# Kernel tuning notes

Hardware: AMD Instinct MI355X
Metric: run time of the kernel (lower is better)

Reference implementation:

```python
import jax, jax.numpy as jnp
import numpy as np

HEADS = 8
GROUPS = 8  # min(8, ch)
EPS = 1e-5


def group_norm(x, gamma, beta):
    # x: (B, C, H, W); normalize over (C/G, H, W) per group
    B, C, H, W = x.shape
    xg = x.reshape(B, GROUPS, C // GROUPS, H, W)
    mu = jnp.mean(xg, axis=(2, 3, 4), keepdims=True)
    var = jnp.var(xg, axis=(2, 3, 4), keepdims=True)
    xn = ((xg - mu) * jax.lax.rsqrt(var + EPS)).reshape(B, C, H, W)
    return xn * gamma[None, :, None, None] + beta[None, :, None, None]


def setup_inputs() -> dict:
    key = jax.random.key(0)
    k1, k2, k3 = jax.random.split(key, 3)
    B, C, H, W = 8, 512, 32, 32
    x = jax.random.normal(k1, (B, C, H, W), dtype=jnp.float32)
    gn_gamma = jnp.ones((C,), dtype=jnp.float32)
    gn_beta = jnp.zeros((C,), dtype=jnp.float32)
    # conv1x1 weights, torch shape (out,in,1,1) squeezed to (out,in)
    w_qkv = jax.random.normal(k2, (3 * C, C), dtype=jnp.float32) * (1.0 / np.sqrt(C))
    w_proj = jax.random.normal(k3, (C, C), dtype=jnp.float32) * (1.0 / np.sqrt(C))
    b_proj = jnp.zeros((C,), dtype=jnp.float32)
    return {"x": x, "gn_gamma": gn_gamma, "gn_beta": gn_beta,
            "w_qkv": w_qkv, "w_proj": w_proj, "b_proj": b_proj}


def reference(x, gn_gamma, gn_beta, w_qkv, w_proj, b_proj):
    B, C, H, W = x.shape
    hd = C // HEADS  # head_dim
    N = H * W
    xn = group_norm(x, gn_gamma, gn_beta)
    # 1x1 conv == channel matmul: (B,3C,H,W)
    qkv = jnp.einsum('oc,bchw->bohw', w_qkv, xn)
    q, k, v = jnp.split(qkv, 3, axis=1)

    def sh(t):  # (B,C,H,W) -> (B, heads, N, head_dim)
        return t.reshape(B, HEADS, hd, N).transpose(0, 1, 3, 2)

    q, k, v = sh(q), sh(k), sh(v)
    scale = hd ** -0.5
    attn = jax.nn.softmax(jnp.einsum('bhnd,bhmd->bhnm', q, k) * scale, axis=-1)
    out = jnp.einsum('bhnm,bhmd->bhnd', attn, v)  # (B,heads,N,hd)
    out = out.transpose(0, 1, 3, 2).reshape(B, C, H, W)
    proj = jnp.einsum('oc,bchw->bohw', w_proj, out) + b_proj[None, :, None, None]
    return x + proj
```

## Files before the change

### kernel.cpp

```cpp
#include <hip/hip_runtime.h>
#include <cstdint>


typedef __bf16 bf16_t;
typedef bf16_t bf16x8 __attribute__((ext_vector_type(8)));
typedef float f32x4 __attribute__((ext_vector_type(4)));

__device__ __forceinline__ uint16_t f2bf(float f) {
  uint32_t x = __builtin_bit_cast(uint32_t, f);
  x += 0x7FFFu + ((x >> 16) & 1u);
  return (uint16_t)(x >> 16);
}
__device__ __forceinline__ bf16x8 frag_ld(const uint16_t* p) {
  return __builtin_bit_cast(bf16x8, *(const uint4*)p);
}
__device__ __forceinline__ void gl_lds16(const uint16_t* g, uint16_t* l) {
  __builtin_amdgcn_global_load_lds(
      (const __attribute__((address_space(1))) uint32_t*)g,
      (__attribute__((address_space(3))) uint32_t*)l, 16, 0, 0);
}
#define MFMA16(a, b, c) __builtin_amdgcn_mfma_f32_16x16x32_bf16((a), (b), (c), 0, 0, 0)

__global__ __launch_bounds__(256) void gnfused_k(const float* __restrict__ wq,
                                                 const float* __restrict__ wp,
                                                 uint16_t* __restrict__ wqb,
                                                 uint16_t* __restrict__ wpb,
                                                 const float* __restrict__ x,
                                                 const float* __restrict__ gamma,
                                                 const float* __restrict__ beta,
                                                 uint16_t* __restrict__ xn) {
  __shared__ alignas(16) float r1[256];
  __shared__ alignas(16) float r2[256];
  __shared__ alignas(16) uint16_t tile[64][72];
  __shared__ float smu, srstd;
  int bx = blockIdx.x, t = threadIdx.x;
  if (bx < 512) {
    int idx = (bx * 256 + t) * 8;
    const float* s;
    uint16_t* d;
    if (idx < 786432) { s = wq + idx; d = wqb + idx; }
    else              { s = wp + (idx - 786432); d = wpb + (idx - 786432); }
    float4 a = *(const float4*)s;
    float4 b = *(const float4*)(s + 4);
    union { uint16_t u[8]; uint4 v; } o;
    o.u[0] = f2bf(a.x); o.u[1] = f2bf(a.y); o.u[2] = f2bf(a.z); o.u[3] = f2bf(a.w);
    o.u[4] = f2bf(b.x); o.u[5] = f2bf(b.y); o.u[6] = f2bf(b.z); o.u[7] = f2bf(b.w);
    *(uint4*)d = o.v;
    return;
  }
  int bg = bx - 512;
  int b = bg >> 3, g = bg & 7;
  const float* xbase = x + (size_t)bg * 65536;

  {
    const float4* p4 = (const float4*)xbase;
    float s1 = 0.f, s2 = 0.f;
    for (int i = t; i < 16384; i += 256) {
      float4 u = p4[i];
      s1 += u.x + u.y + u.z + u.w;
      s2 += u.x * u.x + u.y * u.y + u.z * u.z + u.w * u.w;
    }
    r1[t] = s1; r2[t] = s2; __syncthreads();
    for (int o = 128; o > 0; o >>= 1) {
      if (t < o) { r1[t] += r1[t + o]; r2[t] += r2[t + o]; }
      __syncthreads();
    }
    if (t == 0) {
      float mu = r1[0] * (1.0f / 65536.0f);
      float var = r2[0] * (1.0f / 65536.0f) - mu * mu;
      smu = mu; srstd = rsqrtf(var + 1e-5f);
    }
    __syncthreads();
  }
  float mu = smu, rstd = srstd;

  int c_loc = t >> 2, nch = (t & 3) * 16;
  int c = g * 64 + c_loc;
  float gm = gamma[c], bt = beta[c];
  const float* srcc = xbase + (size_t)c_loc * 1024;
  int n_loc = t >> 2, c0 = (t & 3) * 16;
  uint16_t* dstc = xn + (size_t)b * 524288 + g * 64 + c0;
  for (int nt = 0; nt < 16; nt++) {
    int n0 = nt * 64;
    {
      const float* src = srcc + n0 + nch;
#pragma unroll
      for (int hh = 0; hh < 2; hh++) {
        float4 u0 = *(const float4*)(src + hh * 8);
        float4 u1 = *(const float4*)(src + hh * 8 + 4);
        union { uint16_t u16[8]; uint4 v; } o;
        o.u16[0] = f2bf((u0.x - mu) * rstd * gm + bt);
        o.u16[1] = f2bf((u0.y - mu) * rstd * gm + bt);
        o.u16[2] = f2bf((u0.z - mu) * rstd * gm + bt);
        o.u16[3] = f2bf((u0.w - mu) * rstd * gm + bt);
        o.u16[4] = f2bf((u1.x - mu) * rstd * gm + bt);
        o.u16[5] = f2bf((u1.y - mu) * rstd * gm + bt);
        o.u16[6] = f2bf((u1.z - mu) * rstd * gm + bt);
        o.u16[7] = f2bf((u1.w - mu) * rstd * gm + bt);
        *(uint4*)&tile[c_loc][nch + hh * 8] = o.v;
      }
    }
    __syncthreads();
    {
      union { uint16_t u16[16]; uint4 v[2]; } o;
#pragma unroll
      for (int j = 0; j < 16; j++) o.u16[j] = tile[c0 + j][n_loc];
      uint16_t* dst = dstc + (size_t)(n0 + n_loc) * 512;
      *(uint4*)dst = o.v[0];
      *(uint4*)(dst + 8) = o.v[1];
    }
    __syncthreads();
  }
}

template <int MODE>
__device__ __forceinline__ void gemm_body(uint16_t* Sh,
                                          const uint16_t* Arow, const uint16_t* Brow,
                                          uint16_t* O0, uint16_t* O1,
                                          int b, int n0, int o0) {
  uint16_t* As = Sh;
  uint16_t* Bs = Sh + 8192;
  int t = threadIdx.x;
  int lane = t & 63, w = t >> 6;
  int qd = lane >> 4, l15 = lane & 15;
  int wm = w & 1, wn = w >> 1;

  const uint16_t* gA[4];
  const uint16_t* gB[4];
  uint16_t* lA[4];
  uint16_t* lB[4];
#pragma unroll
  for (int i = 0; i < 4; i++) {
    int p = i * 256 + t;
    int row = p >> 3, slot = p & 7, gc = slot ^ (row & 7);
    gA[i] = Arow + (size_t)row * 512 + gc * 8;
    gB[i] = Brow + (size_t)row * 512 + gc * 8;
    lA[i] = As + (size_t)(p - lane) * 8;
    lB[i] = Bs + (size_t)(p - lane) * 8;
  }

  f32x4 acc[4][4] = {};

  for (int k0 = 0; k0 < 512; k0 += 64) {
    __syncthreads();
#pragma unroll
    for (int i = 0; i < 4; i++) { gl_lds16(gA[i] + k0, lA[i]); gl_lds16(gB[i] + k0, lB[i]); }
    __syncthreads();

#pragma unroll
    for (int h = 0; h < 2; h++) {
      int slot = (h * 4 + qd) ^ (l15 & 7);
      bf16x8 af[4], bfr[4];
#pragma unroll
      for (int mt = 0; mt < 4; mt++)
        af[mt] = frag_ld(As + (wm * 64 + mt * 16 + l15) * 64 + slot * 8);
#pragma unroll
      for (int nt2 = 0; nt2 < 4; nt2++)
        bfr[nt2] = frag_ld(Bs + (wn * 64 + nt2 * 16 + l15) * 64 + slot * 8);
#pragma unroll
      for (int mt = 0; mt < 4; mt++)
#pragma unroll
        for (int nt2 = 0; nt2 < 4; nt2++)
          acc[mt][nt2] = MFMA16(af[mt], bfr[nt2], acc[mt][nt2]);
    }
  }

  __syncthreads();
  uint16_t* buf = Sh + w * 1152;
  float sc = 1.0f;
  uint16_t* gbase;
  size_t rstride;
  int coff;
  if constexpr (MODE == 0) {
    int oc = o0 + wn * 64;
    int hh;
    uint16_t* db;
    if (oc < 512) { db = O0; hh = oc >> 6; sc = 0.125f; }
    else          { db = O1; hh = (oc - 512) >> 6; }
    gbase = db + (size_t)(b * 8 + hh) * 65536 + (size_t)(n0 + wm * 64) * 64;
    rstride = 64;  coff = 0;
  } else {
    gbase = O0 + (size_t)b * 524288 + (size_t)(o0 + wm * 64) * 1024;
    rstride = 1024; coff = n0 + wn * 64;
  }
  int jrow = lane >> 3, joff = (lane & 7) * 8;
#pragma unroll
  for (int mt = 0; mt < 4; mt++) {
#pragma unroll
    for (int nt2 = 0; nt2 < 4; nt2++)
#pragma unroll
      for (int r = 0; r < 4; r++)
        buf[(qd * 4 + r) * 72 + nt2 * 16 + l15] = f2bf(acc[mt][nt2][r] * sc);
#pragma unroll
    for (int half = 0; half < 2; half++) {
      int row = jrow + half * 8;
      uint4 v = *(const uint4*)(buf + row * 72 + joff);
      *(uint4*)(gbase + (size_t)(mt * 16 + row) * rstride + coff + joff) = v;
    }
  }
}

__global__ __launch_bounds__(256) void gemm01_k(const uint16_t* __restrict__ xn,
                                                const uint16_t* __restrict__ wqb,
                                                uint16_t* __restrict__ qtw,
                                                uint16_t* __restrict__ ktw,
                                                uint16_t* __restrict__ vtw) {
  __shared__ alignas(16) uint16_t Sh[16384];
  int id = blockIdx.x;
  int lo = id & 7, hi = id >> 3;
  int o12 = hi % 12, b = hi / 12;
  int n0 = lo * 128;
  if (o12 < 8) {
    int o0 = o12 * 128;
    gemm_body<0>(Sh, xn + (size_t)b * 524288 + (size_t)n0 * 512,
                 wqb + (size_t)o0 * 512, qtw, ktw, b, n0, o0);
  } else {
    int o0 = (o12 - 8) * 128;
    gemm_body<1>(Sh, wqb + (size_t)(1024 + o0) * 512,
                 xn + (size_t)b * 524288 + (size_t)n0 * 512, vtw, nullptr, b, n0, o0);
  }
}

__global__ __launch_bounds__(256) void gemm2_k(const uint16_t* __restrict__ wpb,
                                               const uint16_t* __restrict__ otw,
                                               const float* __restrict__ xres,
                                               const float* __restrict__ biasf,
                                               float* __restrict__ out) {
  __shared__ alignas(16) uint16_t As[2][8192];
  __shared__ alignas(16) uint16_t Bs[2][8192];
  int id = blockIdx.x;
  int lo = id & 7, hi = id >> 3;
  int o0 = (hi & 3) * 128, b = hi >> 2, n0 = lo * 128;
  const uint16_t* Arow = wpb + (size_t)o0 * 512;
  const uint16_t* Brow = otw + (size_t)b * 524288 + (size_t)n0 * 512;

  int t = threadIdx.x, lane = t & 63, w = t >> 6;
  int qd = lane >> 4, l15 = lane & 15;
  int wm = w & 1, wn = w >> 1;

  const uint16_t* gA[4];
  const uint16_t* gB[4];
  int lofs[4];
#pragma unroll
  for (int i = 0; i < 4; i++) {
    int p = i * 256 + t;
    int row = p >> 3, slot = p & 7, gc = slot ^ (row & 7);
    gA[i] = Arow + (size_t)row * 512 + gc * 8;
    gB[i] = Brow + (size_t)row * 512 + gc * 8;
    lofs[i] = (p - lane) * 8;
  }

  f32x4 acc[4][4] = {};
#pragma unroll
  for (int i = 0; i < 4; i++) { gl_lds16(gA[i], &As[0][lofs[i]]); gl_lds16(gB[i], &Bs[0][lofs[i]]); }
  __syncthreads();

  for (int kt = 0; kt < 8; kt++) {
    int cur = kt & 1, nxt = cur ^ 1;
    if (kt < 7) {
      int k0 = (kt + 1) * 64;
#pragma unroll
      for (int i = 0; i < 4; i++) { gl_lds16(gA[i] + k0, &As[nxt][lofs[i]]); gl_lds16(gB[i] + k0, &Bs[nxt][lofs[i]]); }
    }
#pragma unroll
    for (int h = 0; h < 2; h++) {
      int slot = (h * 4 + qd) ^ (l15 & 7);
      bf16x8 af[4], bfr[4];
#pragma unroll
      for (int mt = 0; mt < 4; mt++)
        af[mt] = frag_ld(&As[cur][(wm * 64 + mt * 16 + l15) * 64 + slot * 8]);
#pragma unroll
      for (int nt2 = 0; nt2 < 4; nt2++)
        bfr[nt2] = frag_ld(&Bs[cur][(wn * 64 + nt2 * 16 + l15) * 64 + slot * 8]);
#pragma unroll
      for (int mt = 0; mt < 4; mt++)
#pragma unroll
        for (int nt2 = 0; nt2 < 4; nt2++)
          acc[mt][nt2] = MFMA16(af[mt], bfr[nt2], acc[mt][nt2]);
    }
    __syncthreads();
  }

#pragma unroll
  for (int mt = 0; mt < 4; mt++) {
    int row = wm * 64 + mt * 16 + qd * 4;
#pragma unroll
    for (int nt2 = 0; nt2 < 4; nt2++) {
      int col = wn * 64 + nt2 * 16 + l15;
#pragma unroll
      for (int r = 0; r < 4; r++) {
        int orow = o0 + row + r, n = n0 + col;
        size_t idx = (size_t)b * 524288 + (size_t)orow * 1024 + n;
        out[idx] = xres[idx] + biasf[orow] + acc[mt][nt2][r];
      }
    }
  }
}

__global__ __launch_bounds__(256) void attn_k(const uint16_t* __restrict__ qt,
                                              const uint16_t* __restrict__ ktp,
                                              const uint16_t* __restrict__ vtp,
                                              uint16_t* __restrict__ ot) {
  int bh = blockIdx.x;
  int b = bh >> 3, h = bh & 7;
  int n0 = blockIdx.y * 128;
  const uint16_t* qbase = qt + (size_t)bh * 65536;
  const uint16_t* kbase = ktp + (size_t)bh * 65536;
  const uint16_t* vbase = vtp + (size_t)b * 524288 + (size_t)h * 65536;

  __shared__ alignas(16) uint16_t Ks[2][64 * 64];
  __shared__ alignas(16) uint16_t Vs[2][64 * 64];
  __shared__ alignas(16) uint16_t Ps[128 * 72];

  int t = threadIdx.x, lane = t & 63, w = t >> 6;
  int qd = lane >> 4, l15 = lane & 15;

  bf16x8 qf[2][2];
#pragma unroll
  for (int rs = 0; rs < 2; rs++) {
    const uint16_t* qp = qbase + (size_t)(n0 + w * 32 + rs * 16 + l15) * 64 + qd * 8;
    qf[rs][0] = frag_ld(qp);
    qf[rs][1] = frag_ld(qp + 32);
  }

  int p1 = t, p2 = t + 256;
  int r1 = p1 >> 3, gc1 = (p1 & 7) ^ (r1 & 7);
  int r2 = p2 >> 3, gc2 = (p2 & 7) ^ (r2 & 7);
  const uint16_t* gK1 = kbase + (size_t)r1 * 64 + gc1 * 8;
  const uint16_t* gK2 = kbase + (size_t)r2 * 64 + gc2 * 8;
  const uint16_t* gV1 = vbase + (size_t)r1 * 1024 + gc1 * 8;
  const uint16_t* gV2 = vbase + (size_t)r2 * 1024 + gc2 * 8;
  int lo1 = (p1 - lane) * 8;
  int lo2 = (p2 - lane) * 8;

  f32x4 oaccT[2][4] = {};
  float lsum[2] = {0.f, 0.f};

  gl_lds16(gK1, &Ks[0][lo1]);
  gl_lds16(gK2, &Ks[0][lo2]);
  gl_lds16(gV1, &Vs[0][lo1]);
  gl_lds16(gV2, &Vs[0][lo2]);
  __syncthreads();

  for (int it = 0; it < 16; it++) {
    int cur = it & 1, nxt = cur ^ 1;
    if (it < 15) {
      int m0 = (it + 1) * 64;
      gl_lds16(gK1 + (size_t)m0 * 64, &Ks[nxt][lo1]);
      gl_lds16(gK2 + (size_t)m0 * 64, &Ks[nxt][lo2]);
      gl_lds16(gV1 + m0, &Vs[nxt][lo1]);
      gl_lds16(gV2 + m0, &Vs[nxt][lo2]);
    }
    const uint16_t* Kc = Ks[cur];
    const uint16_t* Vc = Vs[cur];

    f32x4 sacc[2][4] = {};
#pragma unroll
    for (int mt = 0; mt < 4; mt++) {
      int row = mt * 16 + l15;
      int s0 = qd ^ (l15 & 7);
      bf16x8 kf0 = frag_ld(Kc + (size_t)row * 64 + s0 * 8);
      bf16x8 kf1 = frag_ld(Kc + (size_t)row * 64 + (s0 ^ 4) * 8);
#pragma unroll
      for (int rs = 0; rs < 2; rs++) {
        sacc[rs][mt] = MFMA16(kf0, qf[rs][0], sacc[rs][mt]);
        sacc[rs][mt] = MFMA16(kf1, qf[rs][1], sacc[rs][mt]);
      }
    }

#pragma unroll
    for (int rs = 0; rs < 2; rs++)
#pragma unroll
      for (int mt = 0; mt < 4; mt++) {
        union { uint16_t u[4]; uint2 v; } pk;
        float psum = 0.f;
#pragma unroll
        for (int r = 0; r < 4; r++) {
          float p = __expf(sacc[rs][mt][r]);
          psum += p;
          pk.u[r] = (uint16_t)(__builtin_bit_cast(uint32_t, p) >> 16);
        }
        lsum[rs] += psum;
        *(uint2*)(Ps + (size_t)(w * 32 + rs * 16 + l15) * 72 + mt * 16 + qd * 4) = pk.v;
      }

    bf16x8 pf[2][2];
#pragma unroll
    for (int rs = 0; rs < 2; rs++)
#pragma unroll
      for (int ks = 0; ks < 2; ks++)
        pf[rs][ks] = frag_ld(Ps + (size_t)(w * 32 + rs * 16 + l15) * 72 + ks * 32 + qd * 8);
#pragma unroll
    for (int dt = 0; dt < 4; dt++)
#pragma unroll
      for (int ks = 0; ks < 2; ks++) {
        int row = dt * 16 + l15;
        int slot = (ks * 4 + qd) ^ (l15 & 7);
        bf16x8 vf = frag_ld(Vc + (size_t)row * 64 + slot * 8);
#pragma unroll
        for (int rs = 0; rs < 2; rs++)
          oaccT[rs][dt] = MFMA16(vf, pf[rs][ks], oaccT[rs][dt]);
      }

    __syncthreads();
  }

#pragma unroll
  for (int rs = 0; rs < 2; rs++) {
    float s = lsum[rs];
    s += __shfl_xor(s, 16);
    s += __shfl_xor(s, 32);
    float rinv = 1.0f / s;
    int n = n0 + w * 32 + rs * 16 + l15;
    uint16_t* orow = ot + (size_t)b * 524288 + (size_t)n * 512 + h * 64;
#pragma unroll
    for (int dt = 0; dt < 4; dt++) {
      union { uint16_t u[4]; uint2 v; } pk;
#pragma unroll
      for (int r = 0; r < 4; r++) pk.u[r] = f2bf(oaccT[rs][dt][r] * rinv);
      *(uint2*)(orow + dt * 16 + qd * 4) = pk.v;
    }
  }
}

extern "C" void kernel_launch(void* const* d_in, const int* in_sizes, int n_in,
                              void* d_out, int out_size, void* d_ws, size_t ws_size,
                              hipStream_t stream) {
  (void)in_sizes; (void)n_in; (void)out_size; (void)ws_size;
  const float* xf   = (const float*)d_in[0];
  const float* gamf = (const float*)d_in[1];
  const float* betf = (const float*)d_in[2];
  const float* wqf  = (const float*)d_in[3];
  const float* wpf  = (const float*)d_in[4];
  const float* bprf = (const float*)d_in[5];
  float* out = (float*)d_out;

  uint16_t* base = (uint16_t*)d_ws;
  uint16_t* wqb  = base;
  uint16_t* wpb  = wqb + 786432;
  uint16_t* xn   = wpb + 262144;
  uint16_t* qtw  = xn  + 4194304;
  uint16_t* ktw  = qtw + 4194304;
  uint16_t* vtw  = ktw + 4194304;
  uint16_t* otw  = xn;

  gnfused_k<<<576, 256, 0, stream>>>(wqf, wpf, wqb, wpb, xf, gamf, betf, xn);
  gemm01_k<<<768, 256, 0, stream>>>(xn, wqb, qtw, ktw, vtw);
  attn_k<<<dim3(64, 8), 256, 0, stream>>>(qtw, ktw, vtw, otw);
  gemm2_k<<<256, 256, 0, stream>>>(wpb, otw, xf, bprf, out);
}
```

Measured before the change: 168.7 us.

## Split group norm into parallel partial-stats and separate apply kernels

The fused group-norm kernel used only 64 blocks for 64 (batch, group) pairs, each doing a serial stats pass and 16 transpose tiles. The new version computes partial sums over quarter-groups in 256 extra blocks of the prep kernel, writes them to workspace, and a separate 1024-block apply kernel normalizes and transposes one 64x64 tile each. This raises parallelism at the cost of an extra kernel launch, a second read of x, and a small stats buffer.

```diff
diff --git a/kernel.cpp b/kernel.cpp
--- a/kernel.cpp
+++ b/kernel.cpp
@@ -21,18 +21,14 @@
 }
 #define MFMA16(a, b, c) __builtin_amdgcn_mfma_f32_16x16x32_bf16((a), (b), (c), 0, 0, 0)
 
-__global__ __launch_bounds__(256) void gnfused_k(const float* __restrict__ wq,
-                                                 const float* __restrict__ wp,
-                                                 uint16_t* __restrict__ wqb,
-                                                 uint16_t* __restrict__ wpb,
-                                                 const float* __restrict__ x,
-                                                 const float* __restrict__ gamma,
-                                                 const float* __restrict__ beta,
-                                                 uint16_t* __restrict__ xn) {
+__global__ __launch_bounds__(256) void prep_k(const float* __restrict__ wq,
+                                              const float* __restrict__ wp,
+                                              uint16_t* __restrict__ wqb,
+                                              uint16_t* __restrict__ wpb,
+                                              const float* __restrict__ x,
+                                              float* __restrict__ stats) {
   __shared__ alignas(16) float r1[256];
   __shared__ alignas(16) float r2[256];
-  __shared__ alignas(16) uint16_t tile[64][72];
-  __shared__ float smu, srstd;
   int bx = blockIdx.x, t = threadIdx.x;
   if (bx < 512) {
     int idx = (bx * 256 + t) * 8;
@@ -48,68 +44,70 @@
     *(uint4*)d = o.v;
     return;
   }
-  int bg = bx - 512;
-  int b = bg >> 3, g = bg & 7;
-  const float* xbase = x + (size_t)bg * 65536;
-
+  int pg = bx - 512;
+  const float4* p4 = (const float4*)(x + (size_t)(pg >> 2) * 65536 + (pg & 3) * 16384);
+  float s1 = 0.f, s2 = 0.f;
+  for (int i = t; i < 4096; i += 256) {
+    float4 u = p4[i];
+    s1 += u.x + u.y + u.z + u.w;
+    s2 += u.x * u.x + u.y * u.y + u.z * u.z + u.w * u.w;
+  }
+  r1[t] = s1; r2[t] = s2; __syncthreads();
+  for (int o = 128; o > 0; o >>= 1) {
+    if (t < o) { r1[t] += r1[t + o]; r2[t] += r2[t + o]; }
+    __syncthreads();
+  }
+  if (t == 0) { stats[pg * 2] = r1[0]; stats[pg * 2 + 1] = r2[0]; }
+}
+
+__global__ __launch_bounds__(256) void gn_apply_k(const float* __restrict__ x,
+                                                  const float* __restrict__ gamma,
+                                                  const float* __restrict__ beta,
+                                                  const float* __restrict__ stats,
+                                                  uint16_t* __restrict__ xn) {
+  int nt = blockIdx.x, g = blockIdx.y, b = blockIdx.z;
+  int n0 = nt * 64;
+  int bg = b * 8 + g;
+  float s1 = 0.f, s2 = 0.f;
+#pragma unroll
+  for (int p = 0; p < 4; p++) { s1 += stats[(bg * 4 + p) * 2]; s2 += stats[(bg * 4 + p) * 2 + 1]; }
+  float mu   = s1 * (1.0f / 65536.0f);
+  float var  = s2 * (1.0f / 65536.0f) - mu * mu;
+  float rstd = rsqrtf(var + 1e-5f);
+  __shared__ alignas(16) uint16_t tile[64][72];
+  int t = threadIdx.x;
   {
-    const float4* p4 = (const float4*)xbase;
-    float s1 = 0.f, s2 = 0.f;
-    for (int i = t; i < 16384; i += 256) {
-      float4 u = p4[i];
-      s1 += u.x + u.y + u.z + u.w;
-      s2 += u.x * u.x + u.y * u.y + u.z * u.z + u.w * u.w;
-    }
-    r1[t] = s1; r2[t] = s2; __syncthreads();
-    for (int o = 128; o > 0; o >>= 1) {
-      if (t < o) { r1[t] += r1[t + o]; r2[t] += r2[t + o]; }
-      __syncthreads();
-    }
-    if (t == 0) {
-      float mu = r1[0] * (1.0f / 65536.0f);
-      float var = r2[0] * (1.0f / 65536.0f) - mu * mu;
-      smu = mu; srstd = rsqrtf(var + 1e-5f);
-    }
-    __syncthreads();
-  }
-  float mu = smu, rstd = srstd;
-
-  int c_loc = t >> 2, nch = (t & 3) * 16;
-  int c = g * 64 + c_loc;
-  float gm = gamma[c], bt = beta[c];
-  const float* srcc = xbase + (size_t)c_loc * 1024;
-  int n_loc = t >> 2, c0 = (t & 3) * 16;
-  uint16_t* dstc = xn + (size_t)b * 524288 + g * 64 + c0;
-  for (int nt = 0; nt < 16; nt++) {
-    int n0 = nt * 64;
-    {
-      const float* src = srcc + n0 + nch;
-#pragma unroll
-      for (int hh = 0; hh < 2; hh++) {
-        float4 u0 = *(const float4*)(src + hh * 8);
-        float4 u1 = *(const float4*)(src + hh * 8 + 4);
-        union { uint16_t u16[8]; uint4 v; } o;
-        o.u16[0] = f2bf((u0.x - mu) * rstd * gm + bt);
-        o.u16[1] = f2bf((u0.y - mu) * rstd * gm + bt);
-        o.u16[2] = f2bf((u0.z - mu) * rstd * gm + bt);
-        o.u16[3] = f2bf((u0.w - mu) * rstd * gm + bt);
-        o.u16[4] = f2bf((u1.x - mu) * rstd * gm + bt);
-        o.u16[5] = f2bf((u1.y - mu) * rstd * gm + bt);
-        o.u16[6] = f2bf((u1.z - mu) * rstd * gm + bt);
-        o.u16[7] = f2bf((u1.w - mu) * rstd * gm + bt);
-        *(uint4*)&tile[c_loc][nch + hh * 8] = o.v;
-      }
-    }
-    __syncthreads();
-    {
-      union { uint16_t u16[16]; uint4 v[2]; } o;
-#pragma unroll
-      for (int j = 0; j < 16; j++) o.u16[j] = tile[c0 + j][n_loc];
-      uint16_t* dst = dstc + (size_t)(n0 + n_loc) * 512;
-      *(uint4*)dst = o.v[0];
-      *(uint4*)(dst + 8) = o.v[1];
-    }
-    __syncthreads();
+    int c_loc = t >> 2;
+    int nch = (t & 3) * 16;
+    int c = g * 64 + c_loc;
+    float gm = gamma[c], bt = beta[c];
+    const float* src = x + (size_t)b * 524288 + (size_t)c * 1024 + n0 + nch;
+#pragma unroll
+    for (int hh = 0; hh < 2; hh++) {
+      float4 u0 = *(const float4*)(src + hh * 8);
+      float4 u1 = *(const float4*)(src + hh * 8 + 4);
+      union { uint16_t u16[8]; uint4 v; } o;
+      o.u16[0] = f2bf((u0.x - mu) * rstd * gm + bt);
+      o.u16[1] = f2bf((u0.y - mu) * rstd * gm + bt);
+      o.u16[2] = f2bf((u0.z - mu) * rstd * gm + bt);
+      o.u16[3] = f2bf((u0.w - mu) * rstd * gm + bt);
+      o.u16[4] = f2bf((u1.x - mu) * rstd * gm + bt);
+      o.u16[5] = f2bf((u1.y - mu) * rstd * gm + bt);
+      o.u16[6] = f2bf((u1.z - mu) * rstd * gm + bt);
+      o.u16[7] = f2bf((u1.w - mu) * rstd * gm + bt);
+      *(uint4*)&tile[c_loc][nch + hh * 8] = o.v;
+    }
+  }
+  __syncthreads();
+  {
+    int n_loc = t >> 2;
+    int c0 = (t & 3) * 16;
+    union { uint16_t u16[16]; uint4 v[2]; } o;
+#pragma unroll
+    for (int j = 0; j < 16; j++) o.u16[j] = tile[c0 + j][n_loc];
+    uint16_t* dst = xn + (size_t)b * 524288 + (size_t)(n0 + n_loc) * 512 + g * 64 + c0;
+    *(uint4*)dst = o.v[0];
+    *(uint4*)(dst + 8) = o.v[1];
   }
 }
 
@@ -436,7 +434,8 @@
   float* out = (float*)d_out;
 
   uint16_t* base = (uint16_t*)d_ws;
-  uint16_t* wqb  = base;
+  float* stats   = (float*)base;
+  uint16_t* wqb  = base + 1024;
   uint16_t* wpb  = wqb + 786432;
   uint16_t* xn   = wpb + 262144;
   uint16_t* qtw  = xn  + 4194304;
@@ -444,7 +443,8 @@
   uint16_t* vtw  = ktw + 4194304;
   uint16_t* otw  = xn;
 
-  gnfused_k<<<576, 256, 0, stream>>>(wqf, wpf, wqb, wpb, xf, gamf, betf, xn);
+  prep_k<<<768, 256, 0, stream>>>(wqf, wpf, wqb, wpb, xf, stats);
+  gn_apply_k<<<dim3(16, 8, 8), 256, 0, stream>>>(xf, gamf, betf, stats, xn);
   gemm01_k<<<768, 256, 0, stream>>>(xn, wqb, qtw, ktw, vtw);
   attn_k<<<dim3(64, 8), 256, 0, stream>>>(qtw, ktw, vtw, otw);
   gemm2_k<<<256, 256, 0, stream>>>(wpb, otw, xf, bprf, out);
```

Measured after the change: 147.7 us. -12.5%, faster.
